# Optimization experiments

Hardware: AMD Instinct MI355X
Metric: run time of the kernel (lower is better)

The kernel has to match this reference:

```python
import jax, jax.numpy as jnp
import numpy as np

H = 1024
V = 50257
S = 8192


def setup_inputs() -> dict:
    key = jax.random.key(0)
    ks = jax.random.split(key, 13)
    s = 0.02  # param init scale
    return {
        "input": jax.random.randint(ks[0], (1,), 0, V),
        "hidden": jax.random.normal(ks[1], (1, 1, H), jnp.float32),
        "encoder_outputs": jax.random.normal(ks[2], (S, H), jnp.float32),
        "embedding": jax.random.normal(ks[3], (V, H), jnp.float32) * s,
        "attn_w": jax.random.normal(ks[4], (1, 2 * H), jnp.float32) * s,
        "attn_b": jnp.zeros((1,), jnp.float32),
        "comb_w": jax.random.normal(ks[5], (H, 2 * H), jnp.float32) * s,
        "comb_b": jnp.zeros((H,), jnp.float32),
        "w_ih": jax.random.normal(ks[6], (3 * H, H), jnp.float32) * s,
        "w_hh": jax.random.normal(ks[7], (3 * H, H), jnp.float32) * s,
        "b_ih": jnp.zeros((3 * H,), jnp.float32),
        "b_hh": jnp.zeros((3 * H,), jnp.float32),
        "out_w": jax.random.normal(ks[8], (V, H), jnp.float32) * s,
        "out_b": jnp.zeros((V,), jnp.float32),
    }


def reference(input, hidden, encoder_outputs, embedding, attn_w, attn_b,
              comb_w, comb_b, w_ih, w_hh, b_ih, b_hh, out_w, out_b):
    # embedded = embedding(input).view(1,1,-1); dropout in eval mode = identity
    emb = embedding[input[0]]            # [H]
    h0 = hidden[0, 0]                    # [H]
    # Original loop computes the SAME score attn(cat(emb, hidden)) for every
    # timestep -> softmax over a constant vector (uniform weights). Compute the
    # scalar once and broadcast (same math, one GEMV instead of S launches).
    score = jnp.concatenate([emb, h0]) @ attn_w[0] + attn_b[0]   # scalar
    seq_len = encoder_outputs.shape[0]
    attn_weights = jax.nn.softmax(jnp.broadcast_to(score, (seq_len,)))  # [S]
    attn_applied = attn_weights @ encoder_outputs                # [H]
    combined = jnp.concatenate([emb, attn_applied]) @ comb_w.T + comb_b  # [H]
    x = jax.nn.relu(combined)
    # Single GRU step (torch nn.GRU gate math)
    gi = w_ih @ x + b_ih                 # [3H]
    gh = w_hh @ h0 + b_hh                # [3H]
    i_r, i_z, i_n = jnp.split(gi, 3)
    h_r, h_z, h_n = jnp.split(gh, 3)
    r = jax.nn.sigmoid(i_r + h_r)
    z = jax.nn.sigmoid(i_z + h_z)
    n = jnp.tanh(i_n + r * h_n)
    h_new = (1.0 - z) * n + z * h0       # [H]
    logits = h_new @ out_w.T + out_b     # [V]
    output = jax.nn.log_softmax(logits)[None, :]   # [1, V]
    return output, h_new[None, None, :], attn_weights[None, :]
```

## Files before the change

kernel.cpp:

```cpp
#include <hip/hip_runtime.h>
#include <math.h>

#define HN 1024
#define VN 50257
#define SN 8192

#define WS_PARTIAL 0
#define WS_X       8192
#define WS_GH      9216
#define WS_CEMB    12288
#define WS_HNEW    13312
#define WS_LOGITS  14336
#define WS_EXPD    64594

__device__ __forceinline__ float wred(float v) {
#pragma unroll
  for (int m = 32; m; m >>= 1) v += __shfl_xor(v, m);
  return v;
}

__device__ __forceinline__ float dot4(float4 a, float4 b) {
  return a.x * b.x + a.y * b.y + a.z * b.z + a.w * b.w;
}

__global__ __launch_bounds__(1024) void k1_front(
    const float* __restrict__ enc, const int* __restrict__ token,
    const float* __restrict__ embedding, const float* __restrict__ comb_w,
    const float* __restrict__ comb_b, float* __restrict__ ws,
    float* __restrict__ out_attn) {
  const int blk = blockIdx.x, t = threadIdx.x;
  __shared__ float lds[1024];
  const int chunk = blk >> 5, stripe = blk & 31;
  {
    const float* base =
        enc + ((size_t)chunk * 1024 + (t >> 5)) * 1024 + stripe * 32 + (t & 31);
    float s = 0.f;
#pragma unroll 8
    for (int j = 0; j < 32; ++j) s += base[j * 32768];
    lds[t] = s;
  }
  __syncthreads();
  if (t < 32) {
    float a = 0.f;
#pragma unroll
    for (int j = 0; j < 32; ++j) a += lds[t + j * 32];
    ws[WS_PARTIAL + chunk * 1024 + stripe * 32 + t] = a;
    out_attn[blk * 32 + t] = 1.f / 8192.f;
  }
  const int w = t >> 6, l = t & 63;
  if (w < 4) {
    const int i = blk * 4 + w;
    const int tok = token[0];
    const float4* emb4 = (const float4*)embedding + (size_t)tok * 256;
    const float4* cw4 = (const float4*)comb_w + (size_t)i * 512;
    float acc = dot4(cw4[l], emb4[l]) + dot4(cw4[64 + l], emb4[64 + l]) +
                dot4(cw4[128 + l], emb4[128 + l]) + dot4(cw4[192 + l], emb4[192 + l]);
    acc = wred(acc);
    if (l == 0) ws[WS_CEMB + i] = acc + comb_b[i];
  }
}

__global__ __launch_bounds__(1024) void k2_mid(
    const float* __restrict__ w_hh, const float* __restrict__ hidden,
    const float* __restrict__ comb_w, float* __restrict__ ws) {
  const int blk = blockIdx.x, t = threadIdx.x;
  const int w = t >> 6, l = t & 63;
  if (blk < 192) {
    const int r = blk * 16 + w;
    const float4* h4 = (const float4*)hidden;
    const float4* m4 = (const float4*)w_hh + (size_t)r * 256;
    float acc = dot4(m4[l], h4[l]) + dot4(m4[64 + l], h4[64 + l]) +
                dot4(m4[128 + l], h4[128 + l]) + dot4(m4[192 + l], h4[192 + l]);
    acc = wred(acc);
    if (l == 0) ws[WS_GH + r] = acc;
  } else {
    __shared__ float aas[1024];
    float s = 0.f;
#pragma unroll
    for (int j = 0; j < 8; ++j) s += ws[WS_PARTIAL + j * 1024 + t];
    aas[t] = s * (1.f / 8192.f);
    __syncthreads();
    const int i = (blk - 192) * 16 + w;
    const float4* aa4 = (const float4*)aas;
    const float4* cw4 = (const float4*)comb_w + (size_t)i * 512 + 256;
    float acc = dot4(cw4[l], aa4[l]) + dot4(cw4[64 + l], aa4[64 + l]) +
                dot4(cw4[128 + l], aa4[128 + l]) + dot4(cw4[192 + l], aa4[192 + l]);
    acc = wred(acc);
    if (l == 0) ws[WS_X + i] = fmaxf(ws[WS_CEMB + i] + acc, 0.f);
  }
}

__global__ void k4_gates_h(const float* __restrict__ w_ih,
                           const float* __restrict__ b_ih, const float* __restrict__ b_hh,
                           const float* __restrict__ hidden, float* __restrict__ ws,
                           float* __restrict__ d_out) {
  const int w = threadIdx.x >> 6, l = threadIdx.x & 63;
  const int i = blockIdx.x * 4 + w;
  const float4* x4 = (const float4*)(ws + WS_X);
  float4 xv0 = x4[l], xv1 = x4[64 + l], xv2 = x4[128 + l], xv3 = x4[192 + l];
  const float4* m0 = (const float4*)w_ih + (size_t)i * 256;
  const float4* m1 = (const float4*)w_ih + (size_t)(i + 1024) * 256;
  const float4* m2 = (const float4*)w_ih + (size_t)(i + 2048) * 256;
  float a0 = dot4(m0[l], xv0) + dot4(m0[64 + l], xv1) +
             dot4(m0[128 + l], xv2) + dot4(m0[192 + l], xv3);
  float a1 = dot4(m1[l], xv0) + dot4(m1[64 + l], xv1) +
             dot4(m1[128 + l], xv2) + dot4(m1[192 + l], xv3);
  float a2 = dot4(m2[l], xv0) + dot4(m2[64 + l], xv1) +
             dot4(m2[128 + l], xv2) + dot4(m2[192 + l], xv3);
  a0 = wred(a0); a1 = wred(a1); a2 = wred(a2);
  if (l == 0) {
    float ir = a0 + b_ih[i];
    float iz = a1 + b_ih[i + 1024];
    float inn = a2 + b_ih[i + 2048];
    float hr = ws[WS_GH + i] + b_hh[i];
    float hz = ws[WS_GH + i + 1024] + b_hh[i + 1024];
    float hn = ws[WS_GH + i + 2048] + b_hh[i + 2048];
    float rg = 1.f / (1.f + expf(-(ir + hr)));
    float zg = 1.f / (1.f + expf(-(iz + hz)));
    float ng = tanhf(inn + rg * hn);
    float h = (1.f - zg) * ng + zg * hidden[i];
    ws[WS_HNEW + i] = h;
    d_out[VN + i] = h;
  }
}

__global__ void k5_logits(const float* __restrict__ out_w, const float* __restrict__ out_b,
                          float* __restrict__ ws) {
  const int blk = blockIdx.x, t = threadIdx.x;
  const int w = t >> 6, l = t & 63;
  const int gw = blk * 4 + w;
  const float4* h4p = (const float4*)(ws + WS_HNEW);
  float4 h0_ = h4p[l], h1_ = h4p[64 + l], h2_ = h4p[128 + l], h3_ = h4p[192 + l];
  const float4* ow4 = (const float4*)out_w;
  double eacc = 0.0;
  {
    const int v0 = gw, v1 = gw + 8448, v2 = gw + 16896;
    const float4* r0 = ow4 + (size_t)v0 * 256;
    const float4* r1 = ow4 + (size_t)v1 * 256;
    const float4* r2 = ow4 + (size_t)v2 * 256;
    float a0 = dot4(r0[l], h0_) + dot4(r0[64 + l], h1_) +
               dot4(r0[128 + l], h2_) + dot4(r0[192 + l], h3_);
    float a1 = dot4(r1[l], h0_) + dot4(r1[64 + l], h1_) +
               dot4(r1[128 + l], h2_) + dot4(r1[192 + l], h3_);
    float a2 = dot4(r2[l], h0_) + dot4(r2[64 + l], h1_) +
               dot4(r2[128 + l], h2_) + dot4(r2[192 + l], h3_);
    a0 = wred(a0); a1 = wred(a1); a2 = wred(a2);
    if (l == 0) {
      float lg0 = a0 + out_b[v0];
      float lg1 = a1 + out_b[v1];
      float lg2 = a2 + out_b[v2];
      ws[WS_LOGITS + v0] = lg0;
      ws[WS_LOGITS + v1] = lg1;
      ws[WS_LOGITS + v2] = lg2;
      eacc += (double)expf(lg0) + (double)expf(lg1) + (double)expf(lg2);
    }
  }
  {
    const int v0 = gw + 25344, v1 = gw + 33792, v2 = gw + 42240;
    const bool ok2 = (v2 < VN);
    const float4* r0 = ow4 + (size_t)v0 * 256;
    const float4* r1 = ow4 + (size_t)v1 * 256;
    const float4* r2 = ow4 + (size_t)(ok2 ? v2 : v1) * 256;
    float a0 = dot4(r0[l], h0_) + dot4(r0[64 + l], h1_) +
               dot4(r0[128 + l], h2_) + dot4(r0[192 + l], h3_);
    float a1 = dot4(r1[l], h0_) + dot4(r1[64 + l], h1_) +
               dot4(r1[128 + l], h2_) + dot4(r1[192 + l], h3_);
    float a2 = dot4(r2[l], h0_) + dot4(r2[64 + l], h1_) +
               dot4(r2[128 + l], h2_) + dot4(r2[192 + l], h3_);
    a0 = wred(a0); a1 = wred(a1); a2 = wred(a2);
    if (l == 0) {
      float lg0 = a0 + out_b[v0];
      float lg1 = a1 + out_b[v1];
      ws[WS_LOGITS + v0] = lg0;
      ws[WS_LOGITS + v1] = lg1;
      eacc += (double)expf(lg0) + (double)expf(lg1);
      if (ok2) {
        float lg2 = a2 + out_b[v2];
        ws[WS_LOGITS + v2] = lg2;
        eacc += (double)expf(lg2);
      }
    }
  }
  __shared__ double sd[4];
  if (l == 0) sd[w] = eacc;
  __syncthreads();
  if (t == 0) ((double*)(ws + WS_EXPD))[blk] = sd[0] + sd[1] + sd[2] + sd[3];
}

__global__ void k6_final(const float* __restrict__ ws, float* __restrict__ d_out) {
  __shared__ double sd[256];
  const int t = threadIdx.x;
  const double* ed = (const double*)(ws + WS_EXPD);
  double a = 0.0;
#pragma unroll
  for (int j = 0; j < 8; ++j) a += ed[t + j * 256];
  if (t < 64) a += ed[t + 2048];
  sd[t] = a;
  __syncthreads();
  for (int s = 128; s; s >>= 1) {
    if (t < s) sd[t] += sd[t + s];
    __syncthreads();
  }
  const float logZ = (float)log(sd[0]);
  const int v = blockIdx.x * 256 + t;
  if (v < VN) d_out[v] = ws[WS_LOGITS + v] - logZ;
}

extern "C" void kernel_launch(void* const* d_in, const int* in_sizes, int n_in,
                              void* d_out, int out_size, void* d_ws, size_t ws_size,
                              hipStream_t stream) {
  const int* token = (const int*)d_in[0];
  const float* hidden = (const float*)d_in[1];
  const float* enc = (const float*)d_in[2];
  const float* embedding = (const float*)d_in[3];
  const float* comb_w = (const float*)d_in[6];
  const float* comb_b = (const float*)d_in[7];
  const float* w_ih = (const float*)d_in[8];
  const float* w_hh = (const float*)d_in[9];
  const float* b_ih = (const float*)d_in[10];
  const float* b_hh = (const float*)d_in[11];
  const float* out_w = (const float*)d_in[12];
  const float* out_b = (const float*)d_in[13];
  float* out = (float*)d_out;
  float* ws = (float*)d_ws;

  k1_front<<<256, 1024, 0, stream>>>(enc, token, embedding, comb_w, comb_b,
                                     ws, out + VN + HN);
  k2_mid<<<256, 1024, 0, stream>>>(w_hh, hidden, comb_w, ws);
  k4_gates_h<<<256, 256, 0, stream>>>(w_ih, b_ih, b_hh, hidden, ws, out);
  k5_logits<<<2112, 256, 0, stream>>>(out_w, out_b, ws);
  k6_final<<<197, 256, 0, stream>>>(ws, out);
}
```

Baseline: 57.93 us.

## Vectorize encoder column-sum loads and give each logits wave contiguous rows

The encoder column-sum in k1 now uses float4 loads with 8 rows per thread and a shared-memory tree reduction, replacing scalar loads over 32 strided rows. This cuts the number of load instructions and deepens memory-level parallelism, at the cost of more __syncthreads steps. In k5, each wave now computes six consecutive vocabulary rows instead of six rows spaced across the whole matrix, so neighbouring waves read contiguous memory. All six row loads are issued before the reductions, and out-of-range rows are clamped and their results discarded.

```diff
diff --git a/kernel.cpp b/kernel.cpp
--- a/kernel.cpp
+++ b/kernel.cpp
@@ -23,30 +23,45 @@
   return a.x * b.x + a.y * b.y + a.z * b.z + a.w * b.w;
 }
 
+__device__ __forceinline__ float4 f4add(float4 a, float4 b) {
+  return make_float4(a.x + b.x, a.y + b.y, a.z + b.z, a.w + b.w);
+}
+
 __global__ __launch_bounds__(1024) void k1_front(
     const float* __restrict__ enc, const int* __restrict__ token,
     const float* __restrict__ embedding, const float* __restrict__ comb_w,
     const float* __restrict__ comb_b, float* __restrict__ ws,
     float* __restrict__ out_attn) {
   const int blk = blockIdx.x, t = threadIdx.x;
-  __shared__ float lds[1024];
+  __shared__ float4 lds4[1024];
   const int chunk = blk >> 5, stripe = blk & 31;
   {
-    const float* base =
-        enc + ((size_t)chunk * 1024 + (t >> 5)) * 1024 + stripe * 32 + (t & 31);
-    float s = 0.f;
-#pragma unroll 8
-    for (int j = 0; j < 32; ++j) s += base[j * 32768];
-    lds[t] = s;
-  }
-  __syncthreads();
-  if (t < 32) {
-    float a = 0.f;
-#pragma unroll
-    for (int j = 0; j < 32; ++j) a += lds[t + j * 32];
-    ws[WS_PARTIAL + chunk * 1024 + stripe * 32 + t] = a;
-    out_attn[blk * 32 + t] = 1.f / 8192.f;
-  }
+    const int slot = t >> 3, col4 = t & 7;
+    const float4* base = (const float4*)enc +
+                         ((size_t)chunk * 1024 + slot) * 256 + stripe * 8 + col4;
+    float4 acc = make_float4(0.f, 0.f, 0.f, 0.f);
+#pragma unroll
+    for (int j = 0; j < 8; ++j) acc = f4add(acc, base[j * 128 * 256]);
+    lds4[t] = acc;
+  }
+  __syncthreads();
+  if (t < 512) lds4[t] = f4add(lds4[t], lds4[t + 512]);
+  __syncthreads();
+  if (t < 256) lds4[t] = f4add(lds4[t], lds4[t + 256]);
+  __syncthreads();
+  if (t < 128) lds4[t] = f4add(lds4[t], lds4[t + 128]);
+  __syncthreads();
+  if (t < 64) lds4[t] = f4add(lds4[t], lds4[t + 64]);
+  __syncthreads();
+  if (t < 32) lds4[t] = f4add(lds4[t], lds4[t + 32]);
+  __syncthreads();
+  if (t < 16) lds4[t] = f4add(lds4[t], lds4[t + 16]);
+  __syncthreads();
+  if (t < 8) {
+    float4 s = f4add(lds4[t], lds4[t + 8]);
+    ((float4*)(ws + WS_PARTIAL))[chunk * 256 + stripe * 8 + t] = s;
+  }
+  if (t < 32) out_attn[blk * 32 + t] = 1.f / 8192.f;
   const int w = t >> 6, l = t & 63;
   if (w < 4) {
     const int i = blk * 4 + w;
@@ -129,55 +144,30 @@
   const int blk = blockIdx.x, t = threadIdx.x;
   const int w = t >> 6, l = t & 63;
   const int gw = blk * 4 + w;
+  const int base = gw * 6;
   const float4* h4p = (const float4*)(ws + WS_HNEW);
   float4 h0_ = h4p[l], h1_ = h4p[64 + l], h2_ = h4p[128 + l], h3_ = h4p[192 + l];
   const float4* ow4 = (const float4*)out_w;
+  float a[6];
+#pragma unroll
+  for (int r = 0; r < 6; ++r) {
+    const int v = base + r;
+    const int vc = (v < VN) ? v : (VN - 1);
+    const float4* p = ow4 + (size_t)vc * 256;
+    a[r] = dot4(p[l], h0_) + dot4(p[64 + l], h1_) +
+           dot4(p[128 + l], h2_) + dot4(p[192 + l], h3_);
+  }
+#pragma unroll
+  for (int r = 0; r < 6; ++r) a[r] = wred(a[r]);
   double eacc = 0.0;
-  {
-    const int v0 = gw, v1 = gw + 8448, v2 = gw + 16896;
-    const float4* r0 = ow4 + (size_t)v0 * 256;
-    const float4* r1 = ow4 + (size_t)v1 * 256;
-    const float4* r2 = ow4 + (size_t)v2 * 256;
-    float a0 = dot4(r0[l], h0_) + dot4(r0[64 + l], h1_) +
-               dot4(r0[128 + l], h2_) + dot4(r0[192 + l], h3_);
-    float a1 = dot4(r1[l], h0_) + dot4(r1[64 + l], h1_) +
-               dot4(r1[128 + l], h2_) + dot4(r1[192 + l], h3_);
-    float a2 = dot4(r2[l], h0_) + dot4(r2[64 + l], h1_) +
-               dot4(r2[128 + l], h2_) + dot4(r2[192 + l], h3_);
-    a0 = wred(a0); a1 = wred(a1); a2 = wred(a2);
-    if (l == 0) {
-      float lg0 = a0 + out_b[v0];
-      float lg1 = a1 + out_b[v1];
-      float lg2 = a2 + out_b[v2];
-      ws[WS_LOGITS + v0] = lg0;
-      ws[WS_LOGITS + v1] = lg1;
-      ws[WS_LOGITS + v2] = lg2;
-      eacc += (double)expf(lg0) + (double)expf(lg1) + (double)expf(lg2);
-    }
-  }
-  {
-    const int v0 = gw + 25344, v1 = gw + 33792, v2 = gw + 42240;
-    const bool ok2 = (v2 < VN);
-    const float4* r0 = ow4 + (size_t)v0 * 256;
-    const float4* r1 = ow4 + (size_t)v1 * 256;
-    const float4* r2 = ow4 + (size_t)(ok2 ? v2 : v1) * 256;
-    float a0 = dot4(r0[l], h0_) + dot4(r0[64 + l], h1_) +
-               dot4(r0[128 + l], h2_) + dot4(r0[192 + l], h3_);
-    float a1 = dot4(r1[l], h0_) + dot4(r1[64 + l], h1_) +
-               dot4(r1[128 + l], h2_) + dot4(r1[192 + l], h3_);
-    float a2 = dot4(r2[l], h0_) + dot4(r2[64 + l], h1_) +
-               dot4(r2[128 + l], h2_) + dot4(r2[192 + l], h3_);
-    a0 = wred(a0); a1 = wred(a1); a2 = wred(a2);
-    if (l == 0) {
-      float lg0 = a0 + out_b[v0];
-      float lg1 = a1 + out_b[v1];
-      ws[WS_LOGITS + v0] = lg0;
-      ws[WS_LOGITS + v1] = lg1;
-      eacc += (double)expf(lg0) + (double)expf(lg1);
-      if (ok2) {
-        float lg2 = a2 + out_b[v2];
-        ws[WS_LOGITS + v2] = lg2;
-        eacc += (double)expf(lg2);
+  if (l == 0) {
+#pragma unroll
+    for (int r = 0; r < 6; ++r) {
+      const int v = base + r;
+      if (v < VN) {
+        float lg = a[r] + out_b[v];
+        ws[WS_LOGITS + v] = lg;
+        eacc += (double)expf(lg);
       }
     }
   }
```

Result: no change. 58.81 us (+1.5%).
